# Performance work log

Hardware: AMD Instinct MI355X
Metric: run time of the kernel (lower is better)

Reference implementation:

```python
import jax, jax.numpy as jnp
import numpy as np
from jax import lax

DOWNSAMPLE = 4.0   # downsample_rate
THRESHOLD = 0.7    # score threshold
NMS_RANGE = 3      # maxpool NMS kernel


def setup_inputs() -> dict:
    key = jax.random.key(0)
    k1, k2 = jax.random.split(key)
    radiace_factor = jax.random.uniform(k1, (8, 80, 192, 192), dtype=jnp.float32)  # class heatmap
    box = jax.random.uniform(k2, (8, 4, 192, 192), dtype=jnp.float32)              # [dx, dy, w, h]
    return {"radiace_factor": radiace_factor, "box": box}


def _nms(heat, kernel):
    # max_pool2d(kernel, stride=1, padding=(kernel-1)//2) == SAME window max
    hmax = lax.reduce_window(heat, -jnp.inf, lax.max,
                             (1, 1, kernel, kernel), (1, 1, 1, 1), 'SAME')
    return heat * (hmax == heat).astype(heat.dtype)


def reference(radiace_factor, box):
    B, C, H, W = radiace_factor.shape
    r = jnp.float32(DOWNSAMPLE)

    heat = _nms(radiace_factor, NMS_RANGE)
    score = heat.max(axis=1)               # [B,H,W] max over categories
    mask = score > THRESHOLD               # [B,H,W] kept peaks

    # grid of (x=col, y=row) matching torch.where(inds)[::-1]
    gx, gy = jnp.meshgrid(jnp.arange(W, dtype=jnp.float32),
                          jnp.arange(H, dtype=jnp.float32), indexing='xy')
    grid = jnp.stack([gx, gy], axis=-1)    # [H,W,2]

    b = jnp.moveaxis(box, 1, -1)           # [B,H,W,4] = (dx,dy,w,h)
    center_xy = (grid + b[..., 0:2]) * r   # [B,H,W,2]
    wh = b[..., 2:4] * r

    lim = jnp.array([W * DOWNSAMPLE, H * DOWNSAMPLE], dtype=jnp.float32)
    x1y1 = jnp.clip(center_xy - wh * 0.5, 0.0, lim)
    x2y2 = jnp.clip(center_xy + wh * 0.5, 0.0, lim)
    boxes = jnp.concatenate([x1y1, x2y2 - x1y1], axis=-1)  # [B,H,W,4] (x1,y1,w,h)

    # Dense, jit-friendly equivalent of the per-batch gather: zero-out non-kept
    m = mask[..., None]
    boxes_kept = jnp.where(m, boxes, 0.0)
    scores_kept = jnp.where(mask, score, 0.0)
    center_kept = jnp.where(m, center_xy, 0.0)
    return boxes_kept, mask, scores_kept, center_kept
```

## Files before the change

kernel.cpp:

```cpp
#include <hip/hip_runtime.h>
#include <math.h>


#define BB 8
#define CC 80
#define HH 192
#define WW 192
#define SS 6
#define NPIX (SS*WW)
#define NBPIX (BB*HH*WW)

__global__ __launch_bounds__(512) void fused_kernel(const float* __restrict__ heat,
                                                    const float* __restrict__ box,
                                                    float* __restrict__ out) {
    const int tid  = threadIdx.x;
    const int lane = tid & 63;
    const int wv   = tid >> 6;
    const int yt   = blockIdx.x;
    const int b    = blockIdx.y;
    const int y0   = yt * SS;
    const bool lok = lane < 48;
    const int  col0 = lane * 4;

    __shared__ float red[8][SS][WW];

    float4 sc[SS];
#pragma unroll
    for (int i = 0; i < SS; ++i) sc[i] = make_float4(0.f, 0.f, 0.f, 0.f);

    const int cbase = wv * 10;
    const float NI = -INFINITY;

    for (int k = 0; k < 10; ++k) {
        const int c = cbase + k;
        const float* hp = heat + ((size_t)(b * CC + c) * HH) * WW;
        float4 v[SS + 2];
#pragma unroll
        for (int r = 0; r < SS + 2; ++r) {
            const int  row = y0 - 1 + r;
            const bool ok  = lok && ((unsigned)row < HH);
            v[r] = ok ? *reinterpret_cast<const float4*>(hp + row * WW + col0)
                      : make_float4(NI, NI, NI, NI);
        }
#pragma unroll
        for (int i = 0; i < SS; ++i) {
            const float4 a = v[i], m = v[i + 1], d = v[i + 2];
            float4 vm;
            vm.x = fmaxf(fmaxf(a.x, m.x), d.x);
            vm.y = fmaxf(fmaxf(a.y, m.y), d.y);
            vm.z = fmaxf(fmaxf(a.z, m.z), d.z);
            vm.w = fmaxf(fmaxf(a.w, m.w), d.w);

            float L = __shfl_up(vm.w, 1);
            float R = __shfl_down(vm.x, 1);
            if (lane == 0)  L = NI;
            if (lane >= 47) R = NI;

            float4 hm;
            hm.x = fmaxf(fmaxf(L,    vm.x), vm.y);
            hm.y = fmaxf(fmaxf(vm.x, vm.y), vm.z);
            hm.z = fmaxf(fmaxf(vm.y, vm.z), vm.w);
            hm.w = fmaxf(fmaxf(vm.z, vm.w), R);

            sc[i].x = fmaxf(sc[i].x, (m.x == hm.x) ? m.x : 0.0f);
            sc[i].y = fmaxf(sc[i].y, (m.y == hm.y) ? m.y : 0.0f);
            sc[i].z = fmaxf(sc[i].z, (m.z == hm.z) ? m.z : 0.0f);
            sc[i].w = fmaxf(sc[i].w, (m.w == hm.w) ? m.w : 0.0f);
        }
    }

    const int    pixbase = (b * HH + y0) * WW;
    const float* bp0     = box + (size_t)b * 4 * HH * WW + (size_t)y0 * WW;
    float pdx[3], pdy[3], pw[3], ph[3];
#pragma unroll
    for (int kk = 0; kk < 3; ++kk) {
        const int idx = kk * 512 + tid;
        if (idx < NPIX) {
            pdx[kk] = bp0[idx];
            pdy[kk] = bp0[idx + (size_t)HH * WW];
            pw[kk]  = bp0[idx + (size_t)2 * HH * WW];
            ph[kk]  = bp0[idx + (size_t)3 * HH * WW];
        }
    }

    if (lok) {
#pragma unroll
        for (int i = 0; i < SS; ++i)
            *reinterpret_cast<float4*>(&red[wv][i][col0]) = sc[i];
    }
    __syncthreads();

    float* boxes  = out;
    float* maskp  = out + (size_t)4 * NBPIX;
    float* scorep = out + (size_t)5 * NBPIX;
    float* ctr    = out + (size_t)6 * NBPIX;

    const float* rf = &red[0][0][0];

#pragma unroll
    for (int kk = 0; kk < 3; ++kk) {
        const int idx = kk * 512 + tid;
        if (idx < NPIX) {
            const int row = idx / WW;
            const int x   = idx - row * WW;
            const int y   = y0 + row;

            float s = rf[idx];
#pragma unroll
            for (int w = 1; w < 8; ++w) s = fmaxf(s, rf[w * NPIX + idx]);
            const bool m = s > 0.7f;

            const float cx = ((float)x + pdx[kk]) * 4.0f;
            const float cy = ((float)y + pdy[kk]) * 4.0f;
            const float w4 = pw[kk] * 4.0f;
            const float h4 = ph[kk] * 4.0f;
            const float lim = 768.0f;
            const float x1 = fminf(fmaxf(cx - w4 * 0.5f, 0.0f), lim);
            const float y1 = fminf(fmaxf(cy - h4 * 0.5f, 0.0f), lim);
            const float x2 = fminf(fmaxf(cx + w4 * 0.5f, 0.0f), lim);
            const float y2 = fminf(fmaxf(cy + h4 * 0.5f, 0.0f), lim);

            const int pix = pixbase + idx;

            float4 bo;
            bo.x = m ? x1 : 0.0f;
            bo.y = m ? y1 : 0.0f;
            bo.z = m ? (x2 - x1) : 0.0f;
            bo.w = m ? (y2 - y1) : 0.0f;
            reinterpret_cast<float4*>(boxes)[pix] = bo;

            maskp[pix]  = m ? 1.0f : 0.0f;
            scorep[pix] = m ? s : 0.0f;

            float2 cc;
            cc.x = m ? cx : 0.0f;
            cc.y = m ? cy : 0.0f;
            reinterpret_cast<float2*>(ctr)[pix] = cc;
        }
    }
}

extern "C" void kernel_launch(void* const* d_in, const int* in_sizes, int n_in,
                              void* d_out, int out_size, void* d_ws, size_t ws_size,
                              hipStream_t stream) {
    const float* heat = (const float*)d_in[0];
    const float* box  = (const float*)d_in[1];
    float* out = (float*)d_out;

    dim3 g(HH / SS, BB);
    fused_kernel<<<g, 512, 0, stream>>>(heat, box, out);
}
```

Before: 145.6 us.

## Use 1024-thread blocks with 3 columns per lane to fill all 64 lanes

Doubles the block to 16 waves, so each wave covers 5 channels instead of 10. Each lane now handles 3 columns with float3 loads, so all 64 lanes are active instead of 48. This is meant to raise memory-level parallelism and cut idle lanes. In exchange, the float3 loads are no longer 16-byte aligned and may split into narrower loads, the shared-memory reduction buffer doubles, and the final reduction reads 16 partials instead of 8.

```diff
diff --git a/kernel.cpp b/kernel.cpp
--- a/kernel.cpp
+++ b/kernel.cpp
@@ -9,72 +9,71 @@
 #define SS 6
 #define NPIX (SS*WW)
 #define NBPIX (BB*HH*WW)
+#define NT 1024
+#define NW (NT/64)
+#define CPW (CC/NW)
 
-__global__ __launch_bounds__(512) void fused_kernel(const float* __restrict__ heat,
-                                                    const float* __restrict__ box,
-                                                    float* __restrict__ out) {
+__global__ __launch_bounds__(NT) void fused_kernel(const float* __restrict__ heat,
+                                                   const float* __restrict__ box,
+                                                   float* __restrict__ out) {
     const int tid  = threadIdx.x;
     const int lane = tid & 63;
     const int wv   = tid >> 6;
     const int yt   = blockIdx.x;
     const int b    = blockIdx.y;
     const int y0   = yt * SS;
-    const bool lok = lane < 48;
-    const int  col0 = lane * 4;
+    const int col0 = lane * 3;
 
-    __shared__ float red[8][SS][WW];
+    __shared__ float red[NW][SS][WW];
 
-    float4 sc[SS];
+    float3 sc[SS];
 #pragma unroll
-    for (int i = 0; i < SS; ++i) sc[i] = make_float4(0.f, 0.f, 0.f, 0.f);
+    for (int i = 0; i < SS; ++i) sc[i] = make_float3(0.f, 0.f, 0.f);
 
-    const int cbase = wv * 10;
+    const int cbase = wv * CPW;
     const float NI = -INFINITY;
 
-    for (int k = 0; k < 10; ++k) {
+    for (int k = 0; k < CPW; ++k) {
         const int c = cbase + k;
         const float* hp = heat + ((size_t)(b * CC + c) * HH) * WW;
-        float4 v[SS + 2];
+        float3 v[SS + 2];
 #pragma unroll
         for (int r = 0; r < SS + 2; ++r) {
             const int  row = y0 - 1 + r;
-            const bool ok  = lok && ((unsigned)row < HH);
-            v[r] = ok ? *reinterpret_cast<const float4*>(hp + row * WW + col0)
-                      : make_float4(NI, NI, NI, NI);
+            const bool ok  = (unsigned)row < HH;
+            v[r] = ok ? *reinterpret_cast<const float3*>(hp + row * WW + col0)
+                      : make_float3(NI, NI, NI);
         }
 #pragma unroll
         for (int i = 0; i < SS; ++i) {
-            const float4 a = v[i], m = v[i + 1], d = v[i + 2];
-            float4 vm;
+            const float3 a = v[i], m = v[i + 1], d = v[i + 2];
+            float3 vm;
             vm.x = fmaxf(fmaxf(a.x, m.x), d.x);
             vm.y = fmaxf(fmaxf(a.y, m.y), d.y);
             vm.z = fmaxf(fmaxf(a.z, m.z), d.z);
-            vm.w = fmaxf(fmaxf(a.w, m.w), d.w);
 
-            float L = __shfl_up(vm.w, 1);
+            float L = __shfl_up(vm.z, 1);
             float R = __shfl_down(vm.x, 1);
             if (lane == 0)  L = NI;
-            if (lane >= 47) R = NI;
+            if (lane == 63) R = NI;
 
-            float4 hm;
+            float3 hm;
             hm.x = fmaxf(fmaxf(L,    vm.x), vm.y);
             hm.y = fmaxf(fmaxf(vm.x, vm.y), vm.z);
-            hm.z = fmaxf(fmaxf(vm.y, vm.z), vm.w);
-            hm.w = fmaxf(fmaxf(vm.z, vm.w), R);
+            hm.z = fmaxf(fmaxf(vm.y, vm.z), R);
 
             sc[i].x = fmaxf(sc[i].x, (m.x == hm.x) ? m.x : 0.0f);
             sc[i].y = fmaxf(sc[i].y, (m.y == hm.y) ? m.y : 0.0f);
             sc[i].z = fmaxf(sc[i].z, (m.z == hm.z) ? m.z : 0.0f);
-            sc[i].w = fmaxf(sc[i].w, (m.w == hm.w) ? m.w : 0.0f);
         }
     }
 
     const int    pixbase = (b * HH + y0) * WW;
     const float* bp0     = box + (size_t)b * 4 * HH * WW + (size_t)y0 * WW;
-    float pdx[3], pdy[3], pw[3], ph[3];
+    float pdx[2], pdy[2], pw[2], ph[2];
 #pragma unroll
-    for (int kk = 0; kk < 3; ++kk) {
-        const int idx = kk * 512 + tid;
+    for (int kk = 0; kk < 2; ++kk) {
+        const int idx = kk * NT + tid;
         if (idx < NPIX) {
             pdx[kk] = bp0[idx];
             pdy[kk] = bp0[idx + (size_t)HH * WW];
@@ -83,10 +82,11 @@
         }
     }
 
-    if (lok) {
 #pragma unroll
-        for (int i = 0; i < SS; ++i)
-            *reinterpret_cast<float4*>(&red[wv][i][col0]) = sc[i];
+    for (int i = 0; i < SS; ++i) {
+        red[wv][i][col0]     = sc[i].x;
+        red[wv][i][col0 + 1] = sc[i].y;
+        red[wv][i][col0 + 2] = sc[i].z;
     }
     __syncthreads();
 
@@ -98,8 +98,8 @@
     const float* rf = &red[0][0][0];
 
 #pragma unroll
-    for (int kk = 0; kk < 3; ++kk) {
-        const int idx = kk * 512 + tid;
+    for (int kk = 0; kk < 2; ++kk) {
+        const int idx = kk * NT + tid;
         if (idx < NPIX) {
             const int row = idx / WW;
             const int x   = idx - row * WW;
@@ -107,7 +107,7 @@
 
             float s = rf[idx];
 #pragma unroll
-            for (int w = 1; w < 8; ++w) s = fmaxf(s, rf[w * NPIX + idx]);
+            for (int w = 1; w < NW; ++w) s = fmaxf(s, rf[w * NPIX + idx]);
             const bool m = s > 0.7f;
 
             const float cx = ((float)x + pdx[kk]) * 4.0f;
@@ -148,5 +148,5 @@
     float* out = (float*)d_out;
 
     dim3 g(HH / SS, BB);
-    fused_kernel<<<g, 512, 0, stream>>>(heat, box, out);
+    fused_kernel<<<g, NT, 0, stream>>>(heat, box, out);
 }
```

New measurement: 198.8 us. 1.37x slower.
